# Optimization experiments

Measured on AMD Instinct MI355X. Metric: run time of the kernel, lower is better.

Reference implementation:

```python
import jax, jax.numpy as jnp
import numpy as np

K = 16  # neighbors, matches init k


def _knn_indices(points, k):
    # points: (N, 3) -> idx: (N, k), self excluded
    sq = jnp.sum(points ** 2, axis=-1, keepdims=True)          # (N, 1)
    dist2 = sq + sq.T - 2.0 * (points @ points.T)              # (N, N)
    dist2 = jnp.clip(dist2, 0.0)
    n = points.shape[0]
    diag = jnp.eye(n, dtype=bool)
    dist2 = jnp.where(diag, jnp.inf, dist2)
    _, idx = jax.lax.top_k(-dist2, k)                          # smallest k
    return idx


def _features_single(xyz, normals, k):
    # xyz, normals: (N, 3)
    idx = _knn_indices(xyz, k)                                 # (N, k)
    neighbors = xyz[idx]                                       # (N, k, 3)
    centroid = neighbors.mean(axis=1, keepdims=True)           # (N, 1, 3)
    centered = neighbors - centroid                            # (N, k, 3)
    cov = jnp.einsum('nki,nkj->nij', centered, centered) / max(k - 1, 1)  # (N, 3, 3)
    w, v = jnp.linalg.eigh(cov.astype(jnp.float32))            # ascending
    w = w[:, ::-1].astype(xyz.dtype)                           # descending (N, 3)
    v = v[:, :, ::-1].astype(xyz.dtype)                        # (N, 3, 3)
    pca_normal = v[:, :, 2]                                    # smallest-variance dir
    dot = jnp.sum(pca_normal * normals, axis=-1, keepdims=True)
    pca_normal = pca_normal * jnp.sign(dot)
    consistency = jnp.abs(dot)                                 # (N, 1)
    total_var = jnp.clip(w.sum(axis=-1, keepdims=True), 1e-8)
    curvature = w[:, 2:3] / total_var                          # (N, 1)
    perp = jnp.abs(jnp.sum(centered * pca_normal[:, None, :], axis=-1))  # (N, k)
    roughness = perp.mean(axis=-1, keepdims=True)              # (N, 1)
    return jnp.concatenate([consistency, normals, curvature, roughness], axis=-1)


def setup_inputs() -> dict:
    key = jax.random.key(0)
    k1, k2 = jax.random.split(key)
    B, N = 2, 12288
    xyz = jax.random.normal(k1, (B, N, 3), dtype=jnp.float32)
    nrm = jax.random.normal(k2, (B, N, 3), dtype=jnp.float32)
    nrm = nrm / jnp.linalg.norm(nrm, axis=-1, keepdims=True)   # unit normals
    return {"xyz": xyz, "normals": nrm}


def reference(xyz, normals):
    return jax.vmap(lambda p, n: _features_single(p, n, K))(xyz, normals)
```

## Files before the change

kernel.cpp:

```cpp
#include <hip/hip_runtime.h>


#define NPTS 12288
#define NBATCH 2
#define NQ (NPTS * NBATCH)
#define KNN 16
#define NCH 16
#define CHSZ (NPTS / NCH)
#define MKEEP 8
#define QBLK (NQ / 256)

typedef unsigned long long u64;
typedef unsigned short u16;
typedef unsigned int u32;

#define SWAPU(a, b) { u32 _lo = min(a, b); u32 _hi = max(a, b); a = _lo; b = _hi; }
#define DIST(dst, px, py, pz) { float _dx = Qx - (px); float _dy = Qy - (py); float _dz = Qz - (pz); \
                                dst = fmaf(_dz, _dz, fmaf(_dy, _dy, _dx * _dx)); }
#define KEY(kk, dd, rel) { kk = (__float_as_uint(dd) & 0xFFFFFC00u) | (u32)(rel); }

__device__ __forceinline__ u64 shfl_xor_u64(u64 v, int mask) {
  u32 lo = (u32)v, hi = (u32)(v >> 32);
  lo = (u32)__shfl_xor((int)lo, mask);
  hi = (u32)__shfl_xor((int)hi, mask);
  return ((u64)hi << 32) | lo;
}

__global__ __launch_bounds__(256) void pack_kernel(const float* __restrict__ xyz,
                                                   float* __restrict__ xs,
                                                   float* __restrict__ ys,
                                                   float* __restrict__ zs,
                                                   float4* __restrict__ pts4) {
  int i = blockIdx.x * 256 + threadIdx.x;
  if (i < NQ) {
    float x = xyz[3 * i + 0], y = xyz[3 * i + 1], z = xyz[3 * i + 2];
    xs[i] = x; ys[i] = y; zs[i] = z;
    pts4[i] = make_float4(x, y, z, fmaf(z, z, fmaf(y, y, x * x)));
  }
}

__global__ __launch_bounds__(256) void knn_kernel(const float4* __restrict__ pts4,
                                                  u16* __restrict__ cidx) {
  int bid = blockIdx.x;
  int qb = bid % QBLK;
  int chk = bid / QBLK;
  int q0 = qb * 256;
  int b = q0 / NPTS;
  int base = b * NPTS + chk * CHSZ;
  int q = q0 + threadIdx.x;

  float4 Q = pts4[q];
  float qq = Q.w;
  float m2x = -2.0f * Q.x, m2y = -2.0f * Q.y, m2z = -2.0f * Q.z;

  const float4* cp = pts4 + base;

  u32 r0 = ~0u, r1 = ~0u, r2 = ~0u, r3 = ~0u, r4 = ~0u, r5 = ~0u, r6 = ~0u, r7 = ~0u;

#define SVAL(dst, c) dst = fmaf(m2x, (c).x, fmaf(m2y, (c).y, fmaf(m2z, (c).z, qq + (c).w)));

  float4 a0 = cp[0], a1 = cp[1], a2 = cp[2], a3 = cp[3];
  float4 a4 = cp[4], a5 = cp[5], a6 = cp[6], a7 = cp[7];

#pragma unroll 1
  for (int c0 = 0; c0 < CHSZ; c0 += 8) {
    float4 n0 = cp[c0 + 8], n1 = cp[c0 + 9], n2 = cp[c0 + 10], n3 = cp[c0 + 11];
    float4 n4 = cp[c0 + 12], n5 = cp[c0 + 13], n6 = cp[c0 + 14], n7 = cp[c0 + 15];

    float e0, e1, e2, e3, e4, e5, e6, e7;
    SVAL(e0, a0) SVAL(e1, a1) SVAL(e2, a2) SVAL(e3, a3)
    SVAL(e4, a4) SVAL(e5, a5) SVAL(e6, a6) SVAL(e7, a7)
    u32 d0, d1, d2, d3, d4, d5, d6, d7;
    KEY(d0, e0, c0 + 0); KEY(d1, e1, c0 + 1); KEY(d2, e2, c0 + 2); KEY(d3, e3, c0 + 3);
    KEY(d4, e4, c0 + 4); KEY(d5, e5, c0 + 5); KEY(d6, e6, c0 + 6); KEY(d7, e7, c0 + 7);
    SWAPU(d0, d1) SWAPU(d2, d3) SWAPU(d4, d5) SWAPU(d6, d7)
    SWAPU(d0, d2) SWAPU(d1, d3) SWAPU(d4, d6) SWAPU(d5, d7)
    SWAPU(d1, d2) SWAPU(d5, d6)
    SWAPU(d0, d4) SWAPU(d1, d5) SWAPU(d2, d6) SWAPU(d3, d7)
    SWAPU(d2, d4) SWAPU(d3, d5)
    SWAPU(d1, d2) SWAPU(d3, d4) SWAPU(d5, d6)
    u32 m0 = min(r0, d7), m1 = min(r1, d6), m2 = min(r2, d5), m3 = min(r3, d4);
    u32 m4 = min(r4, d3), m5 = min(r5, d2), m6 = min(r6, d1), m7 = min(r7, d0);
    SWAPU(m0, m4) SWAPU(m1, m5) SWAPU(m2, m6) SWAPU(m3, m7)
    SWAPU(m0, m2) SWAPU(m1, m3) SWAPU(m4, m6) SWAPU(m5, m7)
    SWAPU(m0, m1) SWAPU(m2, m3) SWAPU(m4, m5) SWAPU(m6, m7)
    r0 = m0; r1 = m1; r2 = m2; r3 = m3; r4 = m4; r5 = m5; r6 = m6; r7 = m7;

    a0 = n0; a1 = n1; a2 = n2; a3 = n3; a4 = n4; a5 = n5; a6 = n6; a7 = n7;
  }
#undef SVAL

  u32 cb = (u32)(chk * CHSZ);
  uint4 w;
  w.x = (cb + (r0 & 1023u)) | ((cb + (r1 & 1023u)) << 16);
  w.y = (cb + (r2 & 1023u)) | ((cb + (r3 & 1023u)) << 16);
  w.z = (cb + (r4 & 1023u)) | ((cb + (r5 & 1023u)) << 16);
  w.w = (cb + (r6 & 1023u)) | ((cb + (r7 & 1023u)) << 16);
  *(uint4*)(cidx + (size_t)q * (NCH * MKEEP) + chk * MKEEP) = w;
}

__global__ __launch_bounds__(256) void feat_kernel(const float* __restrict__ xs,
                                                   const float* __restrict__ ys,
                                                   const float* __restrict__ zs,
                                                   const float* __restrict__ normals,
                                                   const u16* __restrict__ cidx,
                                                   float* __restrict__ out) {
  __shared__ u32 selidx[4][16];
  int wid = threadIdx.x >> 6;
  int lane = threadIdx.x & 63;
  int t = blockIdx.x * 4 + wid;
  int b = t / NPTS;
  int qi = t - b * NPTS;
  int bbase = b * NPTS;

  float Qx = xs[t], Qy = ys[t], Qz = zs[t];

  u32 pair = ((const u32*)(cidx + (size_t)t * (NCH * MKEEP)))[lane];
  int ia = (int)(pair & 0xFFFFu);
  int ib = (int)(pair >> 16);
  float dA, dB;
  DIST(dA, xs[bbase + ia], ys[bbase + ia], zs[bbase + ia]);
  DIST(dB, xs[bbase + ib], ys[bbase + ib], zs[bbase + ib]);
  u64 e0 = ((u64)__float_as_uint(dA) << 32) | (u32)ia;
  u64 e1 = ((u64)__float_as_uint(dB) << 32) | (u32)ib;

#pragma unroll
  for (int k = 2; k <= 128; k <<= 1) {
#pragma unroll
    for (int j = k >> 1; j > 0; j >>= 1) {
      if (j >= 2) {
        int h = j >> 1;
        u64 p0 = shfl_xor_u64(e0, h);
        u64 p1 = shfl_xor_u64(e1, h);
        bool wantmin = (((lane & h) == 0) == (((2 * lane) & k) == 0));
        e0 = wantmin ? (p0 < e0 ? p0 : e0) : (p0 > e0 ? p0 : e0);
        e1 = wantmin ? (p1 < e1 ? p1 : e1) : (p1 > e1 ? p1 : e1);
      } else {
        bool asc = (((2 * lane) & k) == 0);
        u64 mn = e0 < e1 ? e0 : e1;
        u64 mx = e0 < e1 ? e1 : e0;
        e0 = asc ? mn : mx;
        e1 = asc ? mx : mn;
      }
    }
  }

  u32 i0 = (u32)e0 & 0xFFFFu;
  u32 i1 = (u32)e1 & 0xFFFFu;
  bool f0 = (int)i0 != qi;
  bool f1 = (int)i1 != qi;
  u64 b0 = __ballot(f0);
  u64 b1 = __ballot(f1);
  u64 lm = lane ? (~0ull >> (64 - lane)) : 0ull;
  int pre0 = __popcll(b0 & lm) + __popcll(b1 & lm);
  int pre1 = pre0 + (f0 ? 1 : 0);
  if (f0 && pre0 < KNN) selidx[wid][pre0] = i0;
  if (f1 && pre1 < KNN) selidx[wid][pre1] = i1;
  __syncthreads();

  int nidx = selidx[wid][lane & 15];
  float px = xs[bbase + nidx];
  float py = ys[bbase + nidx];
  float pz = zs[bbase + nidx];

  float sx = px, sy = py, sz = pz;
  sx += __shfl_xor(sx, 1); sy += __shfl_xor(sy, 1); sz += __shfl_xor(sz, 1);
  sx += __shfl_xor(sx, 2); sy += __shfl_xor(sy, 2); sz += __shfl_xor(sz, 2);
  sx += __shfl_xor(sx, 4); sy += __shfl_xor(sy, 4); sz += __shfl_xor(sz, 4);
  sx += __shfl_xor(sx, 8); sy += __shfl_xor(sy, 8); sz += __shfl_xor(sz, 8);
  const float invK = 1.0f / 16.0f;
  float cx = sx * invK, cy = sy * invK, cz = sz * invK;

  float dx = px - cx, dy = py - cy, dz = pz - cz;
  float c00 = dx * dx, c01 = dx * dy, c02 = dx * dz;
  float c11 = dy * dy, c12 = dy * dz, c22 = dz * dz;
#pragma unroll
  for (int m = 1; m <= 8; m <<= 1) {
    c00 += __shfl_xor(c00, m); c01 += __shfl_xor(c01, m); c02 += __shfl_xor(c02, m);
    c11 += __shfl_xor(c11, m); c12 += __shfl_xor(c12, m); c22 += __shfl_xor(c22, m);
  }
  const float inv15 = 1.0f / 15.0f;
  c00 *= inv15; c01 *= inv15; c02 *= inv15;
  c11 *= inv15; c12 *= inv15; c22 *= inv15;

  double a00 = c00, a01 = c01, a02 = c02, a11 = c11, a12 = c12, a22 = c22;
  double tr = a00 + a11 + a22;
  double qm = tr * (1.0 / 3.0);
  double p1 = a01 * a01 + a02 * a02 + a12 * a12;
  double b00 = a00 - qm, b11 = a11 - qm, b22 = a22 - qm;
  double p2 = b00 * b00 + b11 * b11 + b22 * b22 + 2.0 * p1;
  double lmin = qm;
  if (p2 > 0.0) {
    double p = sqrt(p2 * (1.0 / 6.0));
    double ip = 1.0 / p;
    double q00 = b00 * ip, q01 = a01 * ip, q02 = a02 * ip;
    double q11 = b11 * ip, q12 = a12 * ip, q22 = b22 * ip;
    double det = q00 * (q11 * q22 - q12 * q12) - q01 * (q01 * q22 - q12 * q02) +
                 q02 * (q01 * q12 - q11 * q02);
    double r = 0.5 * det;
    r = r < -1.0 ? -1.0 : (r > 1.0 ? 1.0 : r);
    double phi = acos(r) * (1.0 / 3.0);
    lmin = qm + 2.0 * p * cos(phi + 2.0943951023931953);
  }

  double m00 = a00 - lmin, m11 = a11 - lmin, m22 = a22 - lmin;
  double v0x = a01 * a12 - a02 * m11;
  double v0y = a02 * a01 - m00 * a12;
  double v0z = m00 * m11 - a01 * a01;
  double v1x = a01 * m22 - a02 * a12;
  double v1y = a02 * a02 - m00 * m22;
  double v1z = m00 * a12 - a01 * a02;
  double v2x = m11 * m22 - a12 * a12;
  double v2y = a12 * a02 - a01 * m22;
  double v2z = a01 * a12 - m11 * a02;
  double n0 = v0x * v0x + v0y * v0y + v0z * v0z;
  double n1 = v1x * v1x + v1y * v1y + v1z * v1z;
  double n2 = v2x * v2x + v2y * v2y + v2z * v2z;
  double vx, vy, vz, nn;
  if (n0 >= n1 && n0 >= n2) { vx = v0x; vy = v0y; vz = v0z; nn = n0; }
  else if (n1 >= n2)        { vx = v1x; vy = v1y; vz = v1z; nn = n1; }
  else                      { vx = v2x; vy = v2y; vz = v2z; nn = n2; }
  if (nn < 1e-60) { vx = 0.0; vy = 0.0; vz = 1.0; nn = 1.0; }
  double inn = 1.0 / sqrt(nn);
  float vxf = (float)(vx * inn), vyf = (float)(vy * inn), vzf = (float)(vz * inn);

  float s = fabsf(dx * vxf + dy * vyf + dz * vzf);
  s += __shfl_xor(s, 1);
  s += __shfl_xor(s, 2);
  s += __shfl_xor(s, 4);
  s += __shfl_xor(s, 8);

  if (lane == 0) {
    float nrx = normals[3 * (size_t)t + 0];
    float nry = normals[3 * (size_t)t + 1];
    float nrz = normals[3 * (size_t)t + 2];
    float dot = vxf * nrx + vyf * nry + vzf * nrz;
    float cons = fabsf(dot);
    float trf = c00 + c11 + c22;
    float curv = (float)lmin / fmaxf(trf, 1e-8f);
    float* o = out + (size_t)t * 6;
    o[0] = cons;
    o[1] = nrx;
    o[2] = nry;
    o[3] = nrz;
    o[4] = curv;
    o[5] = s * invK;
  }
}

extern "C" void kernel_launch(void* const* d_in, const int* in_sizes, int n_in,
                              void* d_out, int out_size, void* d_ws, size_t ws_size,
                              hipStream_t stream) {
  const float* xyz = (const float*)d_in[0];
  const float* normals = (const float*)d_in[1];
  float* out = (float*)d_out;

  float* xs = (float*)d_ws;
  float* ys = xs + NQ;
  float* zs = ys + NQ;
  float4* pts4 = (float4*)(zs + NQ);
  u16* cidx = (u16*)(pts4 + NQ + 8);

  pack_kernel<<<NQ / 256, 256, 0, stream>>>(xyz, xs, ys, zs, pts4);
  knn_kernel<<<QBLK * NCH, 256, 0, stream>>>(pts4, cidx);
  feat_kernel<<<NQ / 4, 256, 0, stream>>>(xs, ys, zs, normals, cidx, out);
}
```

Before: 155.3 us.

## Switch feature kernel from one wave per query to one thread per query

The feature kernel now gives each query its own thread instead of a whole 64-lane wave. Each thread merges the 16 chunks of 8 candidates with a per-chunk sorting network and a bitonic merge into a register top-16 list. The covariance, eigen solve and roughness are then computed serially from register arrays. This removes the wave-wide bitonic sort, the shuffles, the shared memory and the barrier, and it stops 48 of 64 lanes from sitting idle. In exchange it raises register pressure, and the neighbor reads now gather scattered addresses per thread with only 96 blocks of parallelism.

After: 145.7 us. 6.2% less time.

```diff
diff --git a/kernel.cpp b/kernel.cpp
--- a/kernel.cpp
+++ b/kernel.cpp
@@ -15,16 +15,11 @@
 typedef unsigned int u32;
 
 #define SWAPU(a, b) { u32 _lo = min(a, b); u32 _hi = max(a, b); a = _lo; b = _hi; }
+#define SWAP64(a, b) { u64 _lo = (a) < (b) ? (a) : (b); u64 _hi = (a) < (b) ? (b) : (a); a = _lo; b = _hi; }
+#define MIN64(a, b) ((a) < (b) ? (a) : (b))
 #define DIST(dst, px, py, pz) { float _dx = Qx - (px); float _dy = Qy - (py); float _dz = Qz - (pz); \
                                 dst = fmaf(_dz, _dz, fmaf(_dy, _dy, _dx * _dx)); }
 #define KEY(kk, dd, rel) { kk = (__float_as_uint(dd) & 0xFFFFFC00u) | (u32)(rel); }
-
-__device__ __forceinline__ u64 shfl_xor_u64(u64 v, int mask) {
-  u32 lo = (u32)v, hi = (u32)(v >> 32);
-  lo = (u32)__shfl_xor((int)lo, mask);
-  hi = (u32)__shfl_xor((int)hi, mask);
-  return ((u64)hi << 32) | lo;
-}
 
 __global__ __launch_bounds__(256) void pack_kernel(const float* __restrict__ xyz,
                                                    float* __restrict__ xs,
@@ -105,79 +100,73 @@
                                                    const float* __restrict__ normals,
                                                    const u16* __restrict__ cidx,
                                                    float* __restrict__ out) {
-  __shared__ u32 selidx[4][16];
-  int wid = threadIdx.x >> 6;
-  int lane = threadIdx.x & 63;
-  int t = blockIdx.x * 4 + wid;
+  int t = blockIdx.x * 256 + threadIdx.x;
   int b = t / NPTS;
   int qi = t - b * NPTS;
   int bbase = b * NPTS;
 
   float Qx = xs[t], Qy = ys[t], Qz = zs[t];
 
-  u32 pair = ((const u32*)(cidx + (size_t)t * (NCH * MKEEP)))[lane];
-  int ia = (int)(pair & 0xFFFFu);
-  int ib = (int)(pair >> 16);
-  float dA, dB;
-  DIST(dA, xs[bbase + ia], ys[bbase + ia], zs[bbase + ia]);
-  DIST(dB, xs[bbase + ib], ys[bbase + ib], zs[bbase + ib]);
-  u64 e0 = ((u64)__float_as_uint(dA) << 32) | (u32)ia;
-  u64 e1 = ((u64)__float_as_uint(dB) << 32) | (u32)ib;
-
-#pragma unroll
-  for (int k = 2; k <= 128; k <<= 1) {
-#pragma unroll
-    for (int j = k >> 1; j > 0; j >>= 1) {
-      if (j >= 2) {
-        int h = j >> 1;
-        u64 p0 = shfl_xor_u64(e0, h);
-        u64 p1 = shfl_xor_u64(e1, h);
-        bool wantmin = (((lane & h) == 0) == (((2 * lane) & k) == 0));
-        e0 = wantmin ? (p0 < e0 ? p0 : e0) : (p0 > e0 ? p0 : e0);
-        e1 = wantmin ? (p1 < e1 ? p1 : e1) : (p1 > e1 ? p1 : e1);
-      } else {
-        bool asc = (((2 * lane) & k) == 0);
-        u64 mn = e0 < e1 ? e0 : e1;
-        u64 mx = e0 < e1 ? e1 : e0;
-        e0 = asc ? mn : mx;
-        e1 = asc ? mx : mn;
+  const uint4* crow = (const uint4*)(cidx + (size_t)t * (NCH * MKEEP));
+
+  u64 run[KNN];
+#pragma unroll
+  for (int i = 0; i < KNN; ++i) run[i] = ~0ULL;
+
+#pragma unroll 1
+  for (int ch = 0; ch < NCH; ++ch) {
+    uint4 w = crow[ch];
+    int ix[8];
+    ix[0] = (int)(w.x & 0xFFFFu); ix[1] = (int)(w.x >> 16);
+    ix[2] = (int)(w.y & 0xFFFFu); ix[3] = (int)(w.y >> 16);
+    ix[4] = (int)(w.z & 0xFFFFu); ix[5] = (int)(w.z >> 16);
+    ix[6] = (int)(w.w & 0xFFFFu); ix[7] = (int)(w.w >> 16);
+    u64 s0, s1, s2, s3, s4, s5, s6, s7;
+#define MK(sv, j) { int _i = ix[j]; float _d; DIST(_d, xs[bbase + _i], ys[bbase + _i], zs[bbase + _i]); \
+                    sv = ((u64)__float_as_uint(_d) << 32) | (u32)_i; if (_i == qi) sv = ~0ULL; }
+    MK(s0, 0) MK(s1, 1) MK(s2, 2) MK(s3, 3) MK(s4, 4) MK(s5, 5) MK(s6, 6) MK(s7, 7)
+#undef MK
+    SWAP64(s0, s1) SWAP64(s2, s3) SWAP64(s4, s5) SWAP64(s6, s7)
+    SWAP64(s0, s2) SWAP64(s1, s3) SWAP64(s4, s6) SWAP64(s5, s7)
+    SWAP64(s1, s2) SWAP64(s5, s6)
+    SWAP64(s0, s4) SWAP64(s1, s5) SWAP64(s2, s6) SWAP64(s3, s7)
+    SWAP64(s2, s4) SWAP64(s3, s5)
+    SWAP64(s1, s2) SWAP64(s3, s4) SWAP64(s5, s6)
+    run[8]  = MIN64(run[8],  s7);
+    run[9]  = MIN64(run[9],  s6);
+    run[10] = MIN64(run[10], s5);
+    run[11] = MIN64(run[11], s4);
+    run[12] = MIN64(run[12], s3);
+    run[13] = MIN64(run[13], s2);
+    run[14] = MIN64(run[14], s1);
+    run[15] = MIN64(run[15], s0);
+#pragma unroll
+    for (int j = 8; j >= 1; j >>= 1) {
+#pragma unroll
+      for (int i = 0; i < KNN; ++i) {
+        if ((i & j) == 0) { SWAP64(run[i], run[i | j]) }
       }
     }
   }
 
-  u32 i0 = (u32)e0 & 0xFFFFu;
-  u32 i1 = (u32)e1 & 0xFFFFu;
-  bool f0 = (int)i0 != qi;
-  bool f1 = (int)i1 != qi;
-  u64 b0 = __ballot(f0);
-  u64 b1 = __ballot(f1);
-  u64 lm = lane ? (~0ull >> (64 - lane)) : 0ull;
-  int pre0 = __popcll(b0 & lm) + __popcll(b1 & lm);
-  int pre1 = pre0 + (f0 ? 1 : 0);
-  if (f0 && pre0 < KNN) selidx[wid][pre0] = i0;
-  if (f1 && pre1 < KNN) selidx[wid][pre1] = i1;
-  __syncthreads();
-
-  int nidx = selidx[wid][lane & 15];
-  float px = xs[bbase + nidx];
-  float py = ys[bbase + nidx];
-  float pz = zs[bbase + nidx];
-
-  float sx = px, sy = py, sz = pz;
-  sx += __shfl_xor(sx, 1); sy += __shfl_xor(sy, 1); sz += __shfl_xor(sz, 1);
-  sx += __shfl_xor(sx, 2); sy += __shfl_xor(sy, 2); sz += __shfl_xor(sz, 2);
-  sx += __shfl_xor(sx, 4); sy += __shfl_xor(sy, 4); sz += __shfl_xor(sz, 4);
-  sx += __shfl_xor(sx, 8); sy += __shfl_xor(sy, 8); sz += __shfl_xor(sz, 8);
+  float nx[KNN], ny[KNN], nz[KNN];
+  float sx = 0.f, sy = 0.f, sz = 0.f;
+#pragma unroll
+  for (int i = 0; i < KNN; ++i) {
+    int ni = (int)(u32)run[i];
+    float px = xs[bbase + ni], py = ys[bbase + ni], pz = zs[bbase + ni];
+    nx[i] = px; ny[i] = py; nz[i] = pz;
+    sx += px; sy += py; sz += pz;
+  }
   const float invK = 1.0f / 16.0f;
   float cx = sx * invK, cy = sy * invK, cz = sz * invK;
 
-  float dx = px - cx, dy = py - cy, dz = pz - cz;
-  float c00 = dx * dx, c01 = dx * dy, c02 = dx * dz;
-  float c11 = dy * dy, c12 = dy * dz, c22 = dz * dz;
-#pragma unroll
-  for (int m = 1; m <= 8; m <<= 1) {
-    c00 += __shfl_xor(c00, m); c01 += __shfl_xor(c01, m); c02 += __shfl_xor(c02, m);
-    c11 += __shfl_xor(c11, m); c12 += __shfl_xor(c12, m); c22 += __shfl_xor(c22, m);
+  float c00 = 0.f, c01 = 0.f, c02 = 0.f, c11 = 0.f, c12 = 0.f, c22 = 0.f;
+#pragma unroll
+  for (int i = 0; i < KNN; ++i) {
+    float dx = nx[i] - cx, dy = ny[i] - cy, dz = nz[i] - cz;
+    c00 += dx * dx; c01 += dx * dy; c02 += dx * dz;
+    c11 += dy * dy; c12 += dy * dz; c22 += dz * dz;
   }
   const float inv15 = 1.0f / 15.0f;
   c00 *= inv15; c01 *= inv15; c02 *= inv15;
@@ -224,28 +213,26 @@
   double inn = 1.0 / sqrt(nn);
   float vxf = (float)(vx * inn), vyf = (float)(vy * inn), vzf = (float)(vz * inn);
 
-  float s = fabsf(dx * vxf + dy * vyf + dz * vzf);
-  s += __shfl_xor(s, 1);
-  s += __shfl_xor(s, 2);
-  s += __shfl_xor(s, 4);
-  s += __shfl_xor(s, 8);
-
-  if (lane == 0) {
-    float nrx = normals[3 * (size_t)t + 0];
-    float nry = normals[3 * (size_t)t + 1];
-    float nrz = normals[3 * (size_t)t + 2];
-    float dot = vxf * nrx + vyf * nry + vzf * nrz;
-    float cons = fabsf(dot);
-    float trf = c00 + c11 + c22;
-    float curv = (float)lmin / fmaxf(trf, 1e-8f);
-    float* o = out + (size_t)t * 6;
-    o[0] = cons;
-    o[1] = nrx;
-    o[2] = nry;
-    o[3] = nrz;
-    o[4] = curv;
-    o[5] = s * invK;
-  }
+  float s = 0.f;
+#pragma unroll
+  for (int i = 0; i < KNN; ++i) {
+    s += fabsf((nx[i] - cx) * vxf + (ny[i] - cy) * vyf + (nz[i] - cz) * vzf);
+  }
+
+  float nrx = normals[3 * (size_t)t + 0];
+  float nry = normals[3 * (size_t)t + 1];
+  float nrz = normals[3 * (size_t)t + 2];
+  float dot = vxf * nrx + vyf * nry + vzf * nrz;
+  float cons = fabsf(dot);
+  float trf = c00 + c11 + c22;
+  float curv = (float)lmin / fmaxf(trf, 1e-8f);
+  float* o = out + (size_t)t * 6;
+  o[0] = cons;
+  o[1] = nrx;
+  o[2] = nry;
+  o[3] = nrz;
+  o[4] = curv;
+  o[5] = s * invK;
 }
 
 extern "C" void kernel_launch(void* const* d_in, const int* in_sizes, int n_in,
@@ -263,5 +250,5 @@
 
   pack_kernel<<<NQ / 256, 256, 0, stream>>>(xyz, xs, ys, zs, pts4);
   knn_kernel<<<QBLK * NCH, 256, 0, stream>>>(pts4, cidx);
-  feat_kernel<<<NQ / 4, 256, 0, stream>>>(xs, ys, zs, normals, cidx, out);
-}
+  feat_kernel<<<NQ / 256, 256, 0, stream>>>(xs, ys, zs, normals, cidx, out);
+}
```
